# Performance work log

Hardware: AMD Instinct MI355X
Metric: run time of the kernel (lower is better)

The kernel has to match this reference:

```python
import jax, jax.numpy as jnp
import numpy as np

H, C = 8, 32          # heads, channels per head; H*C = 256 triggers the LN branch
N_NODES = 30000       # nodes per node type
N_EDGES = 100000      # edges per edge type
N_TYPES = 6           # hardwired edge types (all src = Package_Name)
D_IN = 128            # raw input feature dim (Package_Name stays at 128)
LRELU_SLOPE = 0.2     # PyG GATConv default negative_slope


def _segment_softmax(e, dst, n):
    # softmax of per-edge logits e [E,H] grouped by destination node
    m = jax.ops.segment_max(e, dst, num_segments=n)
    ex = jnp.exp(e - m[dst])
    den = jax.ops.segment_sum(ex, dst, num_segments=n)
    return ex / (den[dst] + 1e-16)


def _gat(x_src, x_tgt, src, dst, Ws, Wd, a_s, a_d, b):
    # bipartite GATConv, concat heads, no self loops, no edge features
    hs = (x_src @ Ws).reshape(-1, H, C)   # [Ns,H,C]
    hd = (x_tgt @ Wd).reshape(-1, H, C)   # [Nt,H,C]
    es = jnp.einsum('nhc,hc->nh', hs, a_s)
    ed = jnp.einsum('nhc,hc->nh', hd, a_d)
    e = jax.nn.leaky_relu(es[src] + ed[dst], negative_slope=LRELU_SLOPE)  # [E,H]
    n = x_tgt.shape[0]
    alpha = _segment_softmax(e, dst, n)                                   # [E,H]
    msg = hs[src] * alpha[:, :, None]                                     # [E,H,C]
    out = jax.ops.segment_sum(msg, dst, num_segments=n).reshape(n, H * C) + b
    return out, alpha


def _ln_relu(x, g, b):
    mu = x.mean(-1, keepdims=True)
    var = ((x - mu) ** 2).mean(-1, keepdims=True)
    return jax.nn.relu((x - mu) / jnp.sqrt(var + 1e-5) * g + b)


def setup_inputs() -> dict:
    key = jax.random.key(0)
    ks = jax.random.split(key, 16)
    s = 0.05
    return {
        'x_pkg': jax.random.normal(ks[0], (N_NODES, D_IN), jnp.float32),
        'x_tgt': jax.random.normal(ks[1], (N_TYPES, N_NODES, D_IN), jnp.float32),
        'edge_index': jax.random.randint(ks[2], (N_TYPES, 2, N_EDGES), 0, N_NODES, jnp.int32),
        'W1_src': jax.random.normal(ks[3], (N_TYPES, D_IN, H * C), jnp.float32) * s,
        'W1_dst': jax.random.normal(ks[4], (N_TYPES, D_IN, H * C), jnp.float32) * s,
        'att1_src': jax.random.normal(ks[5], (N_TYPES, H, C), jnp.float32) * s,
        'att1_dst': jax.random.normal(ks[6], (N_TYPES, H, C), jnp.float32) * s,
        'b1': jnp.zeros((N_TYPES, H * C), jnp.float32),
        'W2_src': jax.random.normal(ks[7], (N_TYPES, D_IN, H * C), jnp.float32) * s,
        'W2_dst': jax.random.normal(ks[8], (N_TYPES, H * C, H * C), jnp.float32) * s,
        'att2_src': jax.random.normal(ks[9], (N_TYPES, H, C), jnp.float32) * s,
        'att2_dst': jax.random.normal(ks[10], (N_TYPES, H, C), jnp.float32) * s,
        'b2': jnp.zeros((N_TYPES, H * C), jnp.float32),
        'gamma': jnp.ones((N_TYPES, H * C), jnp.float32),
        'beta': jnp.zeros((N_TYPES, H * C), jnp.float32),
        'Wc': jax.random.normal(ks[11], (N_TYPES * H * C + D_IN, 1), jnp.float32) * s,
        'bc': jnp.zeros((1,), jnp.float32),
    }


def reference(x_pkg, x_tgt, edge_index, W1_src, W1_dst, att1_src, att1_dst, b1,
              W2_src, W2_dst, att2_src, att2_dst, b2, gamma, beta, Wc, bc):
    def layer(xt, ei, Ws, Wd, a_s, a_d, bb):
        return _gat(x_pkg, xt, ei[0], ei[1], Ws, Wd, a_s, a_d, bb)

    vlayer = jax.vmap(layer, in_axes=(0, 0, 0, 0, 0, 0, 0))

    # layer 1: Package_Name -> each of 6 target types; Package_Name itself unchanged
    out1, _ = vlayer(x_tgt, edge_index, W1_src, W1_dst, att1_src, att1_dst, b1)
    x1 = jax.vmap(_ln_relu)(out1, gamma, beta)   # module reuses ln1 after both layers

    # layer 2: src features are still the raw 128-d Package_Name features
    out2, alpha2 = vlayer(x1, edge_index, W2_src, W2_dst, att2_src, att2_dst, b2)
    x2 = jax.vmap(_ln_relu)(out2, gamma, beta)

    # global mean pool per node type, concat (6 targets then Package_Name), classify
    pooled = jnp.concatenate([x2.mean(axis=1).reshape(-1), x_pkg.mean(axis=0)])
    logits = pooled @ Wc[:, 0] + bc[0]
    return logits, alpha2
```

## Files before the change

kernel.cpp:

```cpp
#include <hip/hip_runtime.h>
#include <hip/hip_bf16.h>
#include <cstddef>

#define N_NODES 30000
#define N_EDGES 100000
#define N_TYPES 6
#define D_IN 128
#define HC 256
#define NH 8
#define CH 32

typedef __attribute__((ext_vector_type(8))) unsigned short ushort8_t;
typedef __attribute__((ext_vector_type(4))) unsigned short ushort4_t;
typedef __attribute__((ext_vector_type(8))) __bf16 bf16x8;
typedef __attribute__((ext_vector_type(4))) float floatx4;

#define FG_GRID (N_NODES / 4)

__device__ inline unsigned short f2bf(float f) {
    unsigned u = __float_as_uint(f);
    u += 0x7fffu + ((u >> 16) & 1u);
    return (unsigned short)(u >> 16);
}
__device__ inline float bf2f(unsigned short u) {
    return __uint_as_float(((unsigned)u) << 16);
}

__global__ void zero4(float4* __restrict__ p, int n4) {
    int g = blockIdx.x * blockDim.x + threadIdx.x;
    if (g < n4) p[g] = make_float4(0.f, 0.f, 0.f, 0.f);
}
__global__ void zero_i(int* __restrict__ p, int n) {
    int g = blockIdx.x * blockDim.x + threadIdx.x;
    if (g < n) p[g] = 0;
}
__global__ void to_bf16(const float* __restrict__ x, unsigned short* __restrict__ o, int n4) {
    int g = blockIdx.x * blockDim.x + threadIdx.x;
    if (g >= n4) return;
    float4 v = ((const float4*)x)[g];
    ushort4_t p;
    p[0] = f2bf(v.x); p[1] = f2bf(v.y); p[2] = f2bf(v.z); p[3] = f2bf(v.w);
    *(ushort4_t*)&o[(size_t)g * 4] = p;
}

__global__ void hist_all(const int* __restrict__ ei, int* __restrict__ counts) {
    int t = blockIdx.y;
    int e = blockIdx.x * 256 + threadIdx.x;
    if (e < N_EDGES)
        atomicAdd(&counts[t * N_NODES + ei[(size_t)t * 2 * N_EDGES + N_EDGES + e]], 1);
}

#define SCAN_T 1024
#define SCAN_C 30
__global__ __launch_bounds__(1024) void scan_all(const int* __restrict__ counts_g,
                                                 int* __restrict__ row_ptr_g,
                                                 int* __restrict__ cursor_g) {
    int t = blockIdx.x;
    const int* counts = counts_g + t * N_NODES;
    int* row_ptr = row_ptr_g + t * (N_NODES + 1);
    int* cursor = cursor_g + t * N_NODES;
    __shared__ int part[SCAN_T];
    int tid = threadIdx.x;
    int base = tid * SCAN_C;
    int loc[SCAN_C];
    int s = 0;
    #pragma unroll
    for (int i = 0; i < SCAN_C; ++i) {
        int idx = base + i;
        int v = (idx < N_NODES) ? counts[idx] : 0;
        loc[i] = s; s += v;
    }
    part[tid] = s;
    __syncthreads();
    int tot = s;
    for (int d = 1; d < SCAN_T; d <<= 1) {
        int v = (tid >= d) ? part[tid - d] : 0;
        __syncthreads();
        part[tid] += v;
        __syncthreads();
    }
    int off = part[tid] - tot;
    #pragma unroll
    for (int i = 0; i < SCAN_C; ++i) {
        int idx = base + i;
        if (idx < N_NODES) { int r = off + loc[i]; row_ptr[idx] = r; cursor[idx] = r; }
    }
    if (tid == SCAN_T - 1) row_ptr[N_NODES] = part[SCAN_T - 1];
}

__global__ void fill_all(const int* __restrict__ ei, int* __restrict__ cursor,
                         int* __restrict__ elist) {
    int t = blockIdx.y;
    int e = blockIdx.x * 256 + threadIdx.x;
    if (e < N_EDGES) {
        const int* src = ei + (size_t)t * 2 * N_EDGES;
        const int* dst = src + N_EDGES;
        int pos = atomicAdd(&cursor[t * N_NODES + dst[e]], 1);
        elist[t * N_EDGES + pos] = src[e];
    }
}

__global__ void att_weight_all(const float* __restrict__ W1d, const float* __restrict__ a1d,
                               const float* __restrict__ W2d, const float* __restrict__ a2d,
                               float* __restrict__ wd1, float* __restrict__ wd2) {
    int g = blockIdx.x * blockDim.x + threadIdx.x;
    const int per_t = (D_IN + HC) * NH;
    if (g >= N_TYPES * per_t) return;
    int t = g / per_t, r = g % per_t;
    if (r < D_IN * NH) {
        int k = r >> 3, h = r & 7;
        const float* wr = W1d + (size_t)t * D_IN * HC + (size_t)k * HC + h * CH;
        const float* ar = a1d + t * HC + h * CH;
        float s = 0.f;
        #pragma unroll
        for (int c = 0; c < CH; ++c) s += wr[c] * ar[c];
        wd1[t * D_IN * NH + h * D_IN + k] = s;
    } else {
        r -= D_IN * NH;
        int k = r >> 3, h = r & 7;
        const float* wr = W2d + (size_t)t * HC * HC + (size_t)k * HC + h * CH;
        const float* ar = a2d + t * HC + h * CH;
        float s = 0.f;
        #pragma unroll
        for (int c = 0; c < CH; ++c) s += wr[c] * ar[c];
        wd2[t * HC * NH + h * HC + k] = s;
    }
}

__global__ __launch_bounds__(256) void ed1_all(const float* __restrict__ x_tgt,
                                               const float* __restrict__ wd1,
                                               float* __restrict__ ed1g) {
    const int t = blockIdx.y;
    const int lane = threadIdx.x & 63;
    const int wv = threadIdx.x >> 6;
    const int n8 = lane >> 3, h = lane & 7;
    const int node = blockIdx.x * 32 + wv * 8 + n8;
    if (node >= N_NODES) return;
    const float* xr = x_tgt + ((size_t)t * N_NODES + node) * D_IN;
    const float* wp = wd1 + t * D_IN * NH + h * D_IN;
    float acc = 0.f;
    #pragma unroll
    for (int k = 0; k < D_IN; k += 4) {
        const float4 x4 = *(const float4*)&xr[k];
        const float4 w4 = *(const float4*)&wp[k];
        acc += x4.x * w4.x + x4.y * w4.y + x4.z * w4.z + x4.w * w4.w;
    }
    ed1g[((size_t)t * N_NODES + node) * NH + h] = acc;
}

__global__ __launch_bounds__(256) void gemm_all(const unsigned short* __restrict__ A,
                                                const float* __restrict__ W1s,
                                                const float* __restrict__ W2s,
                                                const float* __restrict__ att1,
                                                const float* __restrict__ att2,
                                                unsigned short* __restrict__ hs_all,
                                                float* __restrict__ es_all) {
    const int j = blockIdx.z;
    const float* B = (j < 6) ? W1s + (size_t)j * D_IN * HC
                             : W2s + (size_t)(j - 6) * D_IN * HC;
    const float* att = (j < 6) ? att1 + j * HC : att2 + (j - 6) * HC;
    unsigned short* Cp = hs_all + (size_t)j * N_NODES * HC;
    float* e_out = es_all + (size_t)j * N_NODES * NH;

    __shared__ unsigned short As[64 * 40];
    __shared__ unsigned short Bs[64 * 40];

    const int tid = threadIdx.x;
    const int w = tid >> 6;
    const int lane = tid & 63;
    const int col = lane & 15;
    const int quad = lane >> 4;
    const int m0 = blockIdx.x * 64;
    const int n0 = blockIdx.y * 64;

    const int am = tid >> 2;
    const int ak = (tid & 3) * 8;
    const int bk2 = (tid >> 4) * 2;
    const int bn4 = (tid & 15) * 4;

    floatx4 acc[4];
    #pragma unroll
    for (int ct = 0; ct < 4; ++ct) acc[ct] = (floatx4){0.f, 0.f, 0.f, 0.f};

    #pragma unroll
    for (int k0 = 0; k0 < D_IN; k0 += 32) {
        {
            int gm = m0 + am;
            ushort8_t v = (ushort8_t){0, 0, 0, 0, 0, 0, 0, 0};
            if (gm < N_NODES) v = *(const ushort8_t*)&A[(size_t)gm * D_IN + k0 + ak];
            *(ushort8_t*)&As[am * 40 + ak] = v;
        }
        {
            const float4 r0 = *(const float4*)&B[(size_t)(k0 + bk2) * HC + n0 + bn4];
            const float4 r1 = *(const float4*)&B[(size_t)(k0 + bk2 + 1) * HC + n0 + bn4];
            float a0[4] = {r0.x, r0.y, r0.z, r0.w};
            float a1[4] = {r1.x, r1.y, r1.z, r1.w};
            #pragma unroll
            for (int q = 0; q < 4; ++q) {
                unsigned pk = (unsigned)f2bf(a0[q]) | ((unsigned)f2bf(a1[q]) << 16);
                *(unsigned*)&Bs[(bn4 + q) * 40 + bk2] = pk;
            }
        }
        __syncthreads();
        {
            ushort8_t araw = *(const ushort8_t*)&As[(w * 16 + col) * 40 + quad * 8];
            bf16x8 af = __builtin_bit_cast(bf16x8, araw);
            #pragma unroll
            for (int ct = 0; ct < 4; ++ct) {
                ushort8_t braw = *(const ushort8_t*)&Bs[(ct * 16 + col) * 40 + quad * 8];
                bf16x8 bf = __builtin_bit_cast(bf16x8, braw);
                acc[ct] = __builtin_amdgcn_mfma_f32_16x16x32_bf16(af, bf, acc[ct], 0, 0, 0);
            }
        }
        __syncthreads();
    }

    #pragma unroll
    for (int ct = 0; ct < 4; ++ct) {
        #pragma unroll
        for (int r = 0; r < 4; ++r) {
            int gm = m0 + w * 16 + quad * 4 + r;
            if (gm < N_NODES) Cp[(size_t)gm * HC + n0 + ct * 16 + col] = f2bf(acc[ct][r]);
        }
    }

    float attv[4];
    #pragma unroll
    for (int ct = 0; ct < 4; ++ct) attv[ct] = att[n0 + ct * 16 + col];
    const int hbase = n0 >> 5;
    #pragma unroll
    for (int r = 0; r < 4; ++r) {
        float h0v = acc[0][r] * attv[0] + acc[1][r] * attv[1];
        float h1v = acc[2][r] * attv[2] + acc[3][r] * attv[3];
        #pragma unroll
        for (int off = 1; off < 16; off <<= 1) {
            h0v += __shfl_xor(h0v, off);
            h1v += __shfl_xor(h1v, off);
        }
        if (col == 0) {
            int gm = m0 + w * 16 + quad * 4 + r;
            if (gm < N_NODES) {
                e_out[gm * NH + hbase] = h0v;
                e_out[gm * NH + hbase + 1] = h1v;
            }
        }
    }
}

__device__ inline void edge4(const float* __restrict__ es,
                             const unsigned short* __restrict__ hs,
                             int s_pre, int i, int cm,
                             int h_l, int lane, float ed_mine,
                             float& den, float4& acc) {
    const int i1 = (i + 1 < cm) ? i + 1 : cm;
    const int i2 = (i + 2 < cm) ? i + 2 : cm;
    const int i3 = (i + 3 < cm) ? i + 3 : cm;
    const int s0 = __shfl(s_pre, i);
    const int s1 = __shfl(s_pre, i1);
    const int s2 = __shfl(s_pre, i2);
    const int s3 = __shfl(s_pre, i3);
    float q0 = es[s0 * NH + h_l];
    float q1 = es[s1 * NH + h_l];
    float q2 = es[s2 * NH + h_l];
    float q3 = es[s3 * NH + h_l];
    const ushort4_t v0 = *(const ushort4_t*)&hs[(size_t)s0 * HC + lane * 4];
    const ushort4_t v1 = *(const ushort4_t*)&hs[(size_t)s1 * HC + lane * 4];
    const ushort4_t v2 = *(const ushort4_t*)&hs[(size_t)s2 * HC + lane * 4];
    const ushort4_t v3 = *(const ushort4_t*)&hs[(size_t)s3 * HC + lane * 4];
    q0 += ed_mine; q0 = (q0 >= 0.f) ? q0 : 0.2f * q0;
    q1 += ed_mine; q1 = (q1 >= 0.f) ? q1 : 0.2f * q1;
    q2 += ed_mine; q2 = (q2 >= 0.f) ? q2 : 0.2f * q2;
    q3 += ed_mine; q3 = (q3 >= 0.f) ? q3 : 0.2f * q3;
    const float x0 = __expf(q0);
    const float x1 = (i + 1 <= cm) ? __expf(q1) : 0.f;
    const float x2 = (i + 2 <= cm) ? __expf(q2) : 0.f;
    const float x3 = (i + 3 <= cm) ? __expf(q3) : 0.f;
    den += (x0 + x1) + (x2 + x3);
    acc.x += x0 * bf2f(v0[0]) + x1 * bf2f(v1[0]) + x2 * bf2f(v2[0]) + x3 * bf2f(v3[0]);
    acc.y += x0 * bf2f(v0[1]) + x1 * bf2f(v1[1]) + x2 * bf2f(v2[1]) + x3 * bf2f(v3[1]);
    acc.z += x0 * bf2f(v0[2]) + x1 * bf2f(v1[2]) + x2 * bf2f(v2[2]) + x3 * bf2f(v3[2]);
    acc.w += x0 * bf2f(v0[3]) + x1 * bf2f(v1[3]) + x2 * bf2f(v2[3]) + x3 * bf2f(v3[3]);
}

__device__ inline void edge1(const float* __restrict__ es,
                             const unsigned short* __restrict__ hs,
                             int s, int h_l, int lane, float ed_mine,
                             float& den, float4& acc) {
    float x = es[s * NH + h_l] + ed_mine;
    x = (x >= 0.f) ? x : 0.2f * x;
    const float ex = __expf(x);
    den += ex;
    const ushort4_t hv = *(const ushort4_t*)&hs[(size_t)s * HC + lane * 4];
    acc.x += ex * bf2f(hv[0]); acc.y += ex * bf2f(hv[1]);
    acc.z += ex * bf2f(hv[2]); acc.w += ex * bf2f(hv[3]);
}

__global__ __launch_bounds__(256) void fused_gather_all(
        const int* __restrict__ row_ptr_g, const int* __restrict__ elist_g,
        const float* __restrict__ es_all, const float* __restrict__ ed1g,
        const unsigned short* __restrict__ hs_all,
        const float* __restrict__ b1, const float* __restrict__ b2,
        const float* __restrict__ gamma, const float* __restrict__ beta,
        const float* __restrict__ wd2,
        float* __restrict__ ed2g_all, float* __restrict__ deng_all,
        float* __restrict__ ppart) {
    const int t = blockIdx.y;
    const int* row_ptr = row_ptr_g + t * (N_NODES + 1);
    const int* elist = elist_g + t * N_EDGES;
    const float* es1 = es_all + (size_t)t * N_NODES * NH;
    const float* es2 = es_all + (size_t)(6 + t) * N_NODES * NH;
    const unsigned short* hs1 = hs_all + (size_t)t * N_NODES * HC;
    const unsigned short* hs2 = hs_all + (size_t)(6 + t) * N_NODES * HC;
    const float* gam = gamma + t * HC;
    const float* bet = beta + t * HC;
    const float* w2 = wd2 + t * HC * NH;
    float* ed2g = ed2g_all + (size_t)t * N_NODES * NH;
    float* deng = deng_all + (size_t)t * N_NODES * NH;

    const int lane = threadIdx.x & 63;
    const int w = threadIdx.x >> 6;
    const int d = blockIdx.x * 4 + w;
    const int h_l = lane >> 3;

    const float ed_mine = ed1g[((size_t)t * N_NODES + d) * NH + h_l];
    const int e0 = row_ptr[d], e1n = row_ptr[d + 1];
    const int cnt = e1n - e0;
    int s_pre = 0;
    if (lane < cnt) s_pre = elist[e0 + lane];

    float den1 = 0.f, den2 = 0.f;
    float4 acc1 = make_float4(0.f, 0.f, 0.f, 0.f);
    float4 acc2 = make_float4(0.f, 0.f, 0.f, 0.f);

    float q20, q21, q22, q23;
    ushort4_t v20, v21, v22, v23;
    const bool fast = (cnt > 0) && (cnt <= 4);

    if (fast) {
        const int cm = cnt - 1;
        const int s0 = __shfl(s_pre, 0);
        const int s1 = __shfl(s_pre, (1 < cm) ? 1 : cm);
        const int s2 = __shfl(s_pre, (2 < cm) ? 2 : cm);
        const int s3 = __shfl(s_pre, cm);
        float q10 = es1[s0 * NH + h_l];
        float q11 = es1[s1 * NH + h_l];
        float q12 = es1[s2 * NH + h_l];
        float q13 = es1[s3 * NH + h_l];
        const ushort4_t v10 = *(const ushort4_t*)&hs1[(size_t)s0 * HC + lane * 4];
        const ushort4_t v11 = *(const ushort4_t*)&hs1[(size_t)s1 * HC + lane * 4];
        const ushort4_t v12 = *(const ushort4_t*)&hs1[(size_t)s2 * HC + lane * 4];
        const ushort4_t v13 = *(const ushort4_t*)&hs1[(size_t)s3 * HC + lane * 4];
        q20 = es2[s0 * NH + h_l];
        q21 = es2[s1 * NH + h_l];
        q22 = es2[s2 * NH + h_l];
        q23 = es2[s3 * NH + h_l];
        v20 = *(const ushort4_t*)&hs2[(size_t)s0 * HC + lane * 4];
        v21 = *(const ushort4_t*)&hs2[(size_t)s1 * HC + lane * 4];
        v22 = *(const ushort4_t*)&hs2[(size_t)s2 * HC + lane * 4];
        v23 = *(const ushort4_t*)&hs2[(size_t)s3 * HC + lane * 4];
        q10 += ed_mine; q10 = (q10 >= 0.f) ? q10 : 0.2f * q10;
        q11 += ed_mine; q11 = (q11 >= 0.f) ? q11 : 0.2f * q11;
        q12 += ed_mine; q12 = (q12 >= 0.f) ? q12 : 0.2f * q12;
        q13 += ed_mine; q13 = (q13 >= 0.f) ? q13 : 0.2f * q13;
        const float x0 = __expf(q10);
        const float x1 = (cnt > 1) ? __expf(q11) : 0.f;
        const float x2 = (cnt > 2) ? __expf(q12) : 0.f;
        const float x3 = (cnt > 3) ? __expf(q13) : 0.f;
        den1 = (x0 + x1) + (x2 + x3);
        acc1.x = x0 * bf2f(v10[0]) + x1 * bf2f(v11[0]) + x2 * bf2f(v12[0]) + x3 * bf2f(v13[0]);
        acc1.y = x0 * bf2f(v10[1]) + x1 * bf2f(v11[1]) + x2 * bf2f(v12[1]) + x3 * bf2f(v13[1]);
        acc1.z = x0 * bf2f(v10[2]) + x1 * bf2f(v11[2]) + x2 * bf2f(v12[2]) + x3 * bf2f(v13[2]);
        acc1.w = x0 * bf2f(v10[3]) + x1 * bf2f(v11[3]) + x2 * bf2f(v12[3]) + x3 * bf2f(v13[3]);
    } else if (cnt > 0) {
        const int c1 = (cnt < 64) ? cnt : 64;
        const int cm = c1 - 1;
        for (int i = 0; i < c1; i += 4)
            edge4(es1, hs1, s_pre, i, cm, h_l, lane, ed_mine, den1, acc1);
        if (cnt > 64)
            for (int ii = e0 + 64; ii < e1n; ++ii)
                edge1(es1, hs1, elist[ii], h_l, lane, ed_mine, den1, acc1);
    }

    const float inv1 = 1.f / (den1 + 1e-16f);
    const float4 bv1 = *(const float4*)&b1[t * HC + lane * 4];
    acc1.x = acc1.x * inv1 + bv1.x; acc1.y = acc1.y * inv1 + bv1.y;
    acc1.z = acc1.z * inv1 + bv1.z; acc1.w = acc1.w * inv1 + bv1.w;

    float s1 = acc1.x + acc1.y + acc1.z + acc1.w;
    float s2 = acc1.x * acc1.x + acc1.y * acc1.y + acc1.z * acc1.z + acc1.w * acc1.w;
    #pragma unroll
    for (int off = 1; off < 64; off <<= 1) { s1 += __shfl_xor(s1, off); s2 += __shfl_xor(s2, off); }
    const float mu = s1 * (1.f / 256.f);
    const float var = s2 * (1.f / 256.f) - mu * mu;
    const float rstd = rsqrtf(var + 1e-5f);
    const float4 g4 = *(const float4*)&gam[lane * 4];
    const float4 b4 = *(const float4*)&bet[lane * 4];
    const float ya0 = fmaxf((acc1.x - mu) * rstd * g4.x + b4.x, 0.f);
    const float ya1 = fmaxf((acc1.y - mu) * rstd * g4.y + b4.y, 0.f);
    const float ya2 = fmaxf((acc1.z - mu) * rstd * g4.z + b4.z, 0.f);
    const float ya3 = fmaxf((acc1.w - mu) * rstd * g4.w + b4.w, 0.f);

    __shared__ __align__(16) float ya_s[4][256];
    {
        const int c0 = lane * 4;
        const int widx = (c0 & ~31) | ((c0 & 31) ^ ((lane >> 3) << 2));
        *(float4*)&ya_s[w][widx] = make_float4(ya0, ya1, ya2, ya3);
    }
    const int k8 = lane >> 3;
    const int hh = lane & 7;
    const float* w2h = w2 + hh * HC;
    float e2 = 0.f;
    #pragma unroll
    for (int jj = 0; jj < 8; ++jj) {
        const int idx = k8 * 32 + ((jj * 4) ^ (k8 << 2));
        const float4 y = *(const float4*)&ya_s[w][idx];
        const float4 wv = *(const float4*)&w2h[k8 * 32 + jj * 4];
        e2 += y.x * wv.x + y.y * wv.y + y.z * wv.z + y.w * wv.w;
    }
    e2 += __shfl_xor(e2, 8);
    e2 += __shfl_xor(e2, 16);
    e2 += __shfl_xor(e2, 32);
    if (lane < 8) ed2g[d * NH + lane] = e2;
    const float ed2_mine = __shfl(e2, h_l);

    if (fast) {
        q20 += ed2_mine; q20 = (q20 >= 0.f) ? q20 : 0.2f * q20;
        q21 += ed2_mine; q21 = (q21 >= 0.f) ? q21 : 0.2f * q21;
        q22 += ed2_mine; q22 = (q22 >= 0.f) ? q22 : 0.2f * q22;
        q23 += ed2_mine; q23 = (q23 >= 0.f) ? q23 : 0.2f * q23;
        const float x0 = __expf(q20);
        const float x1 = (cnt > 1) ? __expf(q21) : 0.f;
        const float x2 = (cnt > 2) ? __expf(q22) : 0.f;
        const float x3 = (cnt > 3) ? __expf(q23) : 0.f;
        den2 = (x0 + x1) + (x2 + x3);
        acc2.x = x0 * bf2f(v20[0]) + x1 * bf2f(v21[0]) + x2 * bf2f(v22[0]) + x3 * bf2f(v23[0]);
        acc2.y = x0 * bf2f(v20[1]) + x1 * bf2f(v21[1]) + x2 * bf2f(v22[1]) + x3 * bf2f(v23[1]);
        acc2.z = x0 * bf2f(v20[2]) + x1 * bf2f(v21[2]) + x2 * bf2f(v22[2]) + x3 * bf2f(v23[2]);
        acc2.w = x0 * bf2f(v20[3]) + x1 * bf2f(v21[3]) + x2 * bf2f(v22[3]) + x3 * bf2f(v23[3]);
    } else if (cnt > 0) {
        const int c1 = (cnt < 64) ? cnt : 64;
        const int cm = c1 - 1;
        for (int i = 0; i < c1; i += 4)
            edge4(es2, hs2, s_pre, i, cm, h_l, lane, ed2_mine, den2, acc2);
        if (cnt > 64)
            for (int ii = e0 + 64; ii < e1n; ++ii)
                edge1(es2, hs2, elist[ii], h_l, lane, ed2_mine, den2, acc2);
    }

    if ((lane & 7) == 0) deng[d * NH + h_l] = den2;
    const float inv2 = 1.f / (den2 + 1e-16f);
    const float4 bv2 = *(const float4*)&b2[t * HC + lane * 4];
    acc2.x = acc2.x * inv2 + bv2.x; acc2.y = acc2.y * inv2 + bv2.y;
    acc2.z = acc2.z * inv2 + bv2.z; acc2.w = acc2.w * inv2 + bv2.w;

    float t1 = acc2.x + acc2.y + acc2.z + acc2.w;
    float t2 = acc2.x * acc2.x + acc2.y * acc2.y + acc2.z * acc2.z + acc2.w * acc2.w;
    #pragma unroll
    for (int off = 1; off < 64; off <<= 1) { t1 += __shfl_xor(t1, off); t2 += __shfl_xor(t2, off); }
    const float mu2 = t1 * (1.f / 256.f);
    const float var2 = t2 * (1.f / 256.f) - mu2 * mu2;
    const float rstd2 = rsqrtf(var2 + 1e-5f);
    float4 pool;
    pool.x = fmaxf((acc2.x - mu2) * rstd2 * g4.x + b4.x, 0.f);
    pool.y = fmaxf((acc2.y - mu2) * rstd2 * g4.y + b4.y, 0.f);
    pool.z = fmaxf((acc2.z - mu2) * rstd2 * g4.z + b4.z, 0.f);
    pool.w = fmaxf((acc2.w - mu2) * rstd2 * g4.w + b4.w, 0.f);

    __shared__ __align__(16) float sacc[4][260];
    *(float4*)&sacc[w][lane * 4] = pool;
    __syncthreads();
    const int tid = threadIdx.x;
    float tot = sacc[0][tid] + sacc[1][tid] + sacc[2][tid] + sacc[3][tid];
    ppart[((size_t)t * FG_GRID + blockIdx.x) * HC + tid] = tot;
}

__global__ __launch_bounds__(256) void pool_reduce_all(const float* __restrict__ ppart,
                                                       float* __restrict__ psums) {
    int t = blockIdx.y;
    const float* part = ppart + (size_t)t * FG_GRID * HC;
    int tid = threadIdx.x;
    float acc = 0.f;
    for (int b = blockIdx.x; b < FG_GRID; b += gridDim.x)
        acc += part[(size_t)b * HC + tid];
    atomicAdd(&psums[t * HC + tid], acc);
}

__global__ void alpha_all(const int* __restrict__ ei,
                          const float* __restrict__ es_all,
                          const float* __restrict__ ed2g_all,
                          const float* __restrict__ deng_all,
                          float* __restrict__ out) {
    int t = blockIdx.y;
    int g = blockIdx.x * 256 + threadIdx.x;
    if (g >= N_EDGES * NH) return;
    int e = g >> 3, h = g & 7;
    const int* src = ei + (size_t)t * 2 * N_EDGES;
    const int* dst = src + N_EDGES;
    int s = src[e], d = dst[e];
    const float* es = es_all + (size_t)(6 + t) * N_NODES * NH;
    float x = es[s * NH + h] + ed2g_all[(size_t)t * N_NODES * NH + d * NH + h];
    x = (x >= 0.f) ? x : 0.2f * x;
    out[(size_t)t * N_EDGES * NH + g] =
        __expf(x) / (deng_all[(size_t)t * N_NODES * NH + d * NH + h] + 1e-16f);
}

__global__ __launch_bounds__(256) void pkg_accum(const float* __restrict__ x, float* __restrict__ sums) {
    int tid = threadIdx.x;
    int col = tid & 127;
    int rof = tid >> 7;
    float acc = 0.f;
    for (int r = blockIdx.x * 2 + rof; r < N_NODES; r += gridDim.x * 2)
        acc += x[(size_t)r * D_IN + col];
    atomicAdd(&sums[col], acc);
}

__global__ __launch_bounds__(256) void logits_k(const float* __restrict__ psums,
                                                const float* __restrict__ ksums,
                                                const float* __restrict__ Wc,
                                                const float* __restrict__ bc,
                                                float* __restrict__ out) {
    int tid = threadIdx.x;
    const float inv = 1.f / (float)N_NODES;
    float acc = 0.f;
    for (int i = tid; i < N_TYPES * HC; i += 256) acc += psums[i] * inv * Wc[i];
    if (tid < D_IN) acc += ksums[tid] * inv * Wc[N_TYPES * HC + tid];
    #pragma unroll
    for (int off = 32; off; off >>= 1) acc += __shfl_down(acc, off);
    __shared__ float w[4];
    if ((tid & 63) == 0) w[tid >> 6] = acc;
    __syncthreads();
    if (tid == 0) out[0] = w[0] + w[1] + w[2] + w[3] + bc[0];
}

static inline void zf(float* p, int n, hipStream_t stream) {
    int n4 = (n + 3) >> 2;
    zero4<<<(n4 + 255) / 256, 256, 0, stream>>>((float4*)p, n4);
}

extern "C" void kernel_launch(void* const* d_in, const int* in_sizes, int n_in,
                              void* d_out, int out_size, void* d_ws, size_t ws_size,
                              hipStream_t stream) {
    const float* x_pkg    = (const float*)d_in[0];
    const float* x_tgt    = (const float*)d_in[1];
    const int*   ei       = (const int*)d_in[2];
    const float* W1_src   = (const float*)d_in[3];
    const float* W1_dst   = (const float*)d_in[4];
    const float* att1_src = (const float*)d_in[5];
    const float* att1_dst = (const float*)d_in[6];
    const float* b1       = (const float*)d_in[7];
    const float* W2_src   = (const float*)d_in[8];
    const float* W2_dst   = (const float*)d_in[9];
    const float* att2_src = (const float*)d_in[10];
    const float* att2_dst = (const float*)d_in[11];
    const float* b2       = (const float*)d_in[12];
    const float* gamma    = (const float*)d_in[13];
    const float* beta     = (const float*)d_in[14];
    const float* Wc       = (const float*)d_in[15];
    const float* bc       = (const float*)d_in[16];
    float* out = (float*)d_out;

    char* wsb = (char*)d_ws;
    unsigned short* xpkg_bf = (unsigned short*)wsb;
    unsigned short* hs_all  = xpkg_bf + (size_t)N_NODES * D_IN;
    float* es_all   = (float*)(hs_all + (size_t)12 * N_NODES * HC);
    float* ed2g_all = es_all + (size_t)12 * N_NODES * NH;
    float* deng_all = ed2g_all + (size_t)N_TYPES * N_NODES * NH;
    float* psums    = deng_all + (size_t)N_TYPES * N_NODES * NH;
    float* ksums    = psums + N_TYPES * HC;
    float* wd1      = ksums + D_IN;
    float* wd2      = wd1 + N_TYPES * D_IN * NH;
    float* ed1g     = wd2 + N_TYPES * HC * NH;
    float* ppart    = ed1g + (size_t)N_TYPES * N_NODES * NH;
    int* counts  = (int*)(ppart + (size_t)N_TYPES * FG_GRID * HC);
    int* row_ptr = counts + N_TYPES * N_NODES;
    int* cursor  = row_ptr + N_TYPES * (N_NODES + 1);
    int* elist   = cursor + N_TYPES * N_NODES;

    dim3 egrid((N_EDGES + 255) / 256, N_TYPES);

    zf(psums, N_TYPES * HC, stream);
    zf(ksums, D_IN, stream);
    pkg_accum<<<256, 256, 0, stream>>>(x_pkg, ksums);
    {
        int tot = N_TYPES * (D_IN + HC) * NH;
        att_weight_all<<<(tot + 255) / 256, 256, 0, stream>>>(W1_dst, att1_dst, W2_dst, att2_dst, wd1, wd2);
    }
    {
        dim3 g((N_NODES + 31) / 32, N_TYPES);
        ed1_all<<<g, 256, 0, stream>>>(x_tgt, wd1, ed1g);
    }
    to_bf16<<<((N_NODES * D_IN / 4) + 255) / 256, 256, 0, stream>>>(x_pkg, xpkg_bf, N_NODES * D_IN / 4);
    zero_i<<<(N_TYPES * N_NODES + 255) / 256, 256, 0, stream>>>(counts, N_TYPES * N_NODES);
    hist_all<<<egrid, 256, 0, stream>>>(ei, counts);
    scan_all<<<N_TYPES, SCAN_T, 0, stream>>>(counts, row_ptr, cursor);
    fill_all<<<egrid, 256, 0, stream>>>(ei, cursor, elist);

    {
        dim3 g((N_NODES + 63) / 64, HC / 64, 12);
        gemm_all<<<g, 256, 0, stream>>>(xpkg_bf, W1_src, W2_src, att1_src, att2_src,
                                        hs_all, es_all);
    }

    {
        dim3 g(FG_GRID, N_TYPES);
        fused_gather_all<<<g, 256, 0, stream>>>(row_ptr, elist, es_all, ed1g, hs_all,
                                                b1, b2, gamma, beta, wd2,
                                                ed2g_all, deng_all, ppart);
    }
    {
        dim3 g(32, N_TYPES);
        pool_reduce_all<<<g, 256, 0, stream>>>(ppart, psums);
    }
    {
        dim3 g((N_EDGES * NH + 255) / 256, N_TYPES);
        alpha_all<<<g, 256, 0, stream>>>(ei, es_all, ed2g_all, deng_all, out + 1);
    }

    logits_k<<<1, 256, 0, stream>>>(psums, ksums, Wc, bc, out);
}
```

Before: 885.2 us.

## Pretranspose bf16 src weights, load full A tile once, vectorize alpha per edge

Adds a wt_prep kernel that converts and transposes the source projection weights into bf16 [n][k] layout once. The GEMM then stages the whole 64x128 A tile in LDS with a single barrier and reads B fragments straight from global memory, removing the per-k-step conversion and double syncs. The alpha kernel now handles one edge per thread with float4 loads of all 8 heads. The pool reduction grid is doubled. Extra kernel launch and uncached global B reads are the tradeoffs.

Measured after the change: 922.0 us. +4.2%, slower.

```diff
diff --git a/kernel.cpp b/kernel.cpp
--- a/kernel.cpp
+++ b/kernel.cpp
@@ -127,6 +127,35 @@
     }
 }
 
+__global__ __launch_bounds__(256) void wt_prep(const float* __restrict__ W1s,
+                                               const float* __restrict__ W2s,
+                                               unsigned short* __restrict__ Wt) {
+    const int j = blockIdx.z;
+    const float* W = (j < 6) ? W1s + (size_t)j * D_IN * HC
+                             : W2s + (size_t)(j - 6) * D_IN * HC;
+    const int n0 = blockIdx.x * 64;
+    const int k0 = blockIdx.y * 32;
+    __shared__ unsigned short tile[32][71];
+    const int t = threadIdx.x;
+    {
+        const int k = t >> 3, n = (t & 7) * 8;
+        const float4 a = *(const float4*)&W[(size_t)(k0 + k) * HC + n0 + n];
+        const float4 b = *(const float4*)&W[(size_t)(k0 + k) * HC + n0 + n + 4];
+        tile[k][n + 0] = f2bf(a.x); tile[k][n + 1] = f2bf(a.y);
+        tile[k][n + 2] = f2bf(a.z); tile[k][n + 3] = f2bf(a.w);
+        tile[k][n + 4] = f2bf(b.x); tile[k][n + 5] = f2bf(b.y);
+        tile[k][n + 6] = f2bf(b.z); tile[k][n + 7] = f2bf(b.w);
+    }
+    __syncthreads();
+    {
+        const int n = t >> 2, k = (t & 3) * 8;
+        ushort8_t v;
+        #pragma unroll
+        for (int q = 0; q < 8; ++q) v[q] = tile[k + q][n];
+        *(ushort8_t*)&Wt[((size_t)j * HC + n0 + n) * D_IN + k0 + k] = v;
+    }
+}
+
 __global__ __launch_bounds__(256) void ed1_all(const float* __restrict__ x_tgt,
                                                const float* __restrict__ wd1,
                                                float* __restrict__ ed1g) {
@@ -149,21 +178,18 @@
 }
 
 __global__ __launch_bounds__(256) void gemm_all(const unsigned short* __restrict__ A,
-                                                const float* __restrict__ W1s,
-                                                const float* __restrict__ W2s,
+                                                const unsigned short* __restrict__ Wt,
                                                 const float* __restrict__ att1,
                                                 const float* __restrict__ att2,
                                                 unsigned short* __restrict__ hs_all,
                                                 float* __restrict__ es_all) {
     const int j = blockIdx.z;
-    const float* B = (j < 6) ? W1s + (size_t)j * D_IN * HC
-                             : W2s + (size_t)(j - 6) * D_IN * HC;
+    const unsigned short* B = Wt + (size_t)j * HC * D_IN;
     const float* att = (j < 6) ? att1 + j * HC : att2 + (j - 6) * HC;
     unsigned short* Cp = hs_all + (size_t)j * N_NODES * HC;
     float* e_out = es_all + (size_t)j * N_NODES * NH;
 
-    __shared__ unsigned short As[64 * 40];
-    __shared__ unsigned short Bs[64 * 40];
+    __shared__ __align__(16) unsigned short As[64 * 136];
 
     const int tid = threadIdx.x;
     const int w = tid >> 6;
@@ -173,46 +199,33 @@
     const int m0 = blockIdx.x * 64;
     const int n0 = blockIdx.y * 64;
 
-    const int am = tid >> 2;
-    const int ak = (tid & 3) * 8;
-    const int bk2 = (tid >> 4) * 2;
-    const int bn4 = (tid & 15) * 4;
+    {
+        const int r = tid >> 2;
+        const int kc = (tid & 3) * 8;
+        const int gm = m0 + r;
+        #pragma unroll
+        for (int c = 0; c < 4; ++c) {
+            ushort8_t v = (ushort8_t){0, 0, 0, 0, 0, 0, 0, 0};
+            if (gm < N_NODES) v = *(const ushort8_t*)&A[(size_t)gm * D_IN + kc + c * 32];
+            *(ushort8_t*)&As[r * 136 + kc + c * 32] = v;
+        }
+    }
+    __syncthreads();
 
     floatx4 acc[4];
     #pragma unroll
     for (int ct = 0; ct < 4; ++ct) acc[ct] = (floatx4){0.f, 0.f, 0.f, 0.f};
 
     #pragma unroll
-    for (int k0 = 0; k0 < D_IN; k0 += 32) {
-        {
-            int gm = m0 + am;
-            ushort8_t v = (ushort8_t){0, 0, 0, 0, 0, 0, 0, 0};
-            if (gm < N_NODES) v = *(const ushort8_t*)&A[(size_t)gm * D_IN + k0 + ak];
-            *(ushort8_t*)&As[am * 40 + ak] = v;
+    for (int ks = 0; ks < 4; ++ks) {
+        ushort8_t araw = *(const ushort8_t*)&As[(w * 16 + col) * 136 + quad * 8 + ks * 32];
+        bf16x8 af = __builtin_bit_cast(bf16x8, araw);
+        #pragma unroll
+        for (int ct = 0; ct < 4; ++ct) {
+            ushort8_t braw = *(const ushort8_t*)&B[(size_t)(n0 + ct * 16 + col) * D_IN + quad * 8 + ks * 32];
+            bf16x8 bf = __builtin_bit_cast(bf16x8, braw);
+            acc[ct] = __builtin_amdgcn_mfma_f32_16x16x32_bf16(af, bf, acc[ct], 0, 0, 0);
         }
-        {
-            const float4 r0 = *(const float4*)&B[(size_t)(k0 + bk2) * HC + n0 + bn4];
-            const float4 r1 = *(const float4*)&B[(size_t)(k0 + bk2 + 1) * HC + n0 + bn4];
-            float a0[4] = {r0.x, r0.y, r0.z, r0.w};
-            float a1[4] = {r1.x, r1.y, r1.z, r1.w};
-            #pragma unroll
-            for (int q = 0; q < 4; ++q) {
-                unsigned pk = (unsigned)f2bf(a0[q]) | ((unsigned)f2bf(a1[q]) << 16);
-                *(unsigned*)&Bs[(bn4 + q) * 40 + bk2] = pk;
-            }
-        }
-        __syncthreads();
-        {
-            ushort8_t araw = *(const ushort8_t*)&As[(w * 16 + col) * 40 + quad * 8];
-            bf16x8 af = __builtin_bit_cast(bf16x8, araw);
-            #pragma unroll
-            for (int ct = 0; ct < 4; ++ct) {
-                ushort8_t braw = *(const ushort8_t*)&Bs[(ct * 16 + col) * 40 + quad * 8];
-                bf16x8 bf = __builtin_bit_cast(bf16x8, braw);
-                acc[ct] = __builtin_amdgcn_mfma_f32_16x16x32_bf16(af, bf, acc[ct], 0, 0, 0);
-            }
-        }
-        __syncthreads();
     }
 
     #pragma unroll
@@ -485,23 +498,37 @@
     atomicAdd(&psums[t * HC + tid], acc);
 }
 
-__global__ void alpha_all(const int* __restrict__ ei,
+__global__ __launch_bounds__(256) void alpha_all(const int* __restrict__ ei,
                           const float* __restrict__ es_all,
                           const float* __restrict__ ed2g_all,
                           const float* __restrict__ deng_all,
                           float* __restrict__ out) {
     int t = blockIdx.y;
-    int g = blockIdx.x * 256 + threadIdx.x;
-    if (g >= N_EDGES * NH) return;
-    int e = g >> 3, h = g & 7;
+    int e = blockIdx.x * 256 + threadIdx.x;
+    if (e >= N_EDGES) return;
     const int* src = ei + (size_t)t * 2 * N_EDGES;
     const int* dst = src + N_EDGES;
-    int s = src[e], d = dst[e];
-    const float* es = es_all + (size_t)(6 + t) * N_NODES * NH;
-    float x = es[s * NH + h] + ed2g_all[(size_t)t * N_NODES * NH + d * NH + h];
-    x = (x >= 0.f) ? x : 0.2f * x;
-    out[(size_t)t * N_EDGES * NH + g] =
-        __expf(x) / (deng_all[(size_t)t * N_NODES * NH + d * NH + h] + 1e-16f);
+    const int s = src[e], d = dst[e];
+    const float* esp = es_all + (size_t)(6 + t) * N_NODES * NH + (size_t)s * NH;
+    const float* edp = ed2g_all + (size_t)t * N_NODES * NH + (size_t)d * NH;
+    const float* dnp = deng_all + (size_t)t * N_NODES * NH + (size_t)d * NH;
+    const float4 ea = *(const float4*)esp;
+    const float4 eb = *(const float4*)(esp + 4);
+    const float4 da = *(const float4*)edp;
+    const float4 db = *(const float4*)(edp + 4);
+    const float4 na = *(const float4*)dnp;
+    const float4 nb = *(const float4*)(dnp + 4);
+    float x[8];
+    x[0] = ea.x + da.x; x[1] = ea.y + da.y; x[2] = ea.z + da.z; x[3] = ea.w + da.w;
+    x[4] = eb.x + db.x; x[5] = eb.y + db.y; x[6] = eb.z + db.z; x[7] = eb.w + db.w;
+    float n[8] = {na.x, na.y, na.z, na.w, nb.x, nb.y, nb.z, nb.w};
+    float* op = out + (size_t)t * N_EDGES * NH + (size_t)e * NH;
+    #pragma unroll
+    for (int h = 0; h < 8; ++h) {
+        float v = x[h];
+        v = (v >= 0.f) ? v : 0.2f * v;
+        op[h] = __expf(v) / (n[h] + 1e-16f);
+    }
 }
 
 __global__ __launch_bounds__(256) void pkg_accum(const float* __restrict__ x, float* __restrict__ sums) {
@@ -569,7 +596,8 @@
     float* ksums    = psums + N_TYPES * HC;
     float* wd1      = ksums + D_IN;
     float* wd2      = wd1 + N_TYPES * D_IN * NH;
-    float* ed1g     = wd2 + N_TYPES * HC * NH;
+    unsigned short* Wt = (unsigned short*)(wd2 + N_TYPES * HC * NH);
+    float* ed1g     = (float*)(Wt + (size_t)12 * HC * D_IN);
     float* ppart    = ed1g + (size_t)N_TYPES * N_NODES * NH;
     int* counts  = (int*)(ppart + (size_t)N_TYPES * FG_GRID * HC);
     int* row_ptr = counts + N_TYPES * N_NODES;
@@ -586,6 +614,10 @@
         att_weight_all<<<(tot + 255) / 256, 256, 0, stream>>>(W1_dst, att1_dst, W2_dst, att2_dst, wd1, wd2);
     }
     {
+        dim3 g(4, 4, 12);
+        wt_prep<<<g, 256, 0, stream>>>(W1_src, W2_src, Wt);
+    }
+    {
         dim3 g((N_NODES + 31) / 32, N_TYPES);
         ed1_all<<<g, 256, 0, stream>>>(x_tgt, wd1, ed1g);
     }
@@ -597,7 +629,7 @@
 
     {
         dim3 g((N_NODES + 63) / 64, HC / 64, 12);
-        gemm_all<<<g, 256, 0, stream>>>(xpkg_bf, W1_src, W2_src, att1_src, att2_src,
+        gemm_all<<<g, 256, 0, stream>>>(xpkg_bf, Wt, att1_src, att2_src,
                                         hs_all, es_all);
     }
 
@@ -608,11 +640,11 @@
                                                 ed2g_all, deng_all, ppart);
     }
     {
-        dim3 g(32, N_TYPES);
+        dim3 g(64, N_TYPES);
         pool_reduce_all<<<g, 256, 0, stream>>>(ppart, psums);
     }
     {
-        dim3 g((N_EDGES * NH + 255) / 256, N_TYPES);
+        dim3 g((N_EDGES + 255) / 256, N_TYPES);
         alpha_all<<<g, 256, 0, stream>>>(ei, es_all, ed2g_all, deng_all, out + 1);
     }
 
```
